# Performance work log

Hardware: AMD Instinct MI355X
Metric: run time of the kernel (lower is better)

Reference implementation:

```python
import jax, jax.numpy as jnp
import numpy as np

N = 50000
E = 800000
NUM_GRAPHS = 64
D_IN = 261
D_SAGE = 64
D_LIN = 32
N_SAGE_REST = 6
N_LIN_REST = 3
EPS = 1e-5


def _layernorm(x, g, b):
    mu = jnp.mean(x, axis=-1, keepdims=True)
    var = jnp.mean((x - mu) ** 2, axis=-1, keepdims=True)
    return (x - mu) * jax.lax.rsqrt(var + EPS) * g + b


def _sage_block(x, Wl, bl, Wr, g, b, src, dst, inv_deg, residual):
    # mean aggregation of neighbor (source) features onto targets
    msum = jax.ops.segment_sum(x[src], dst, num_segments=N)  # [N, d]
    mean = msum * inv_deg  # [N, d]
    f = mean @ Wl + bl + x @ Wr  # lin_l(aggr) + lin_r(x); lin_r has no bias
    f = jax.nn.gelu(f, approximate=False)
    f = _layernorm(f, g, b)
    if residual:
        f = f + x
    return f


def _lin_block(x, W, b, g, beta, residual):
    f = jax.nn.gelu(x @ W + b, approximate=False)
    f = _layernorm(f, g, beta)
    if residual:
        f = f + x
    return f


def setup_inputs() -> dict:
    key = jax.random.key(0)
    ks = jax.random.split(key, 24)
    x = jax.random.normal(ks[0], (N, D_IN), dtype=jnp.float32)
    edge_index = jax.random.randint(ks[1], (2, E), 0, N, dtype=jnp.int64)
    batch = jnp.sort(jax.random.randint(ks[2], (N,), 0, NUM_GRAPHS, dtype=jnp.int64))

    def glorot(k, shape):
        fan_in = shape[0]
        return jax.random.normal(k, shape, dtype=jnp.float32) / np.sqrt(fan_in)

    inp = {
        "x": x, "edge_index": edge_index, "batch": batch,
        # first SAGE block (261 -> 64, no residual)
        "Wl0": glorot(ks[3], (D_IN, D_SAGE)), "bl0": jnp.zeros((D_SAGE,), jnp.float32),
        "Wr0": glorot(ks[4], (D_IN, D_SAGE)),
        "g0": jnp.ones((D_SAGE,), jnp.float32), "beta0": jnp.zeros((D_SAGE,), jnp.float32),
        # 6 residual SAGE blocks (64 -> 64), stacked
        "Wl": glorot(ks[5], (N_SAGE_REST, D_SAGE, D_SAGE)),
        "bl": jnp.zeros((N_SAGE_REST, D_SAGE), jnp.float32),
        "Wr": glorot(ks[6], (N_SAGE_REST, D_SAGE, D_SAGE)),
        "g": jnp.ones((N_SAGE_REST, D_SAGE), jnp.float32),
        "beta": jnp.zeros((N_SAGE_REST, D_SAGE), jnp.float32),
        # MLP: first LinearBlock 64 -> 32 (no residual)
        "M0": glorot(ks[7], (D_SAGE, D_LIN)), "mb0": jnp.zeros((D_LIN,), jnp.float32),
        "mg0": jnp.ones((D_LIN,), jnp.float32), "mbeta0": jnp.zeros((D_LIN,), jnp.float32),
        # 3 residual LinearBlocks 32 -> 32, stacked
        "M": glorot(ks[8], (N_LIN_REST, D_LIN, D_LIN)),
        "mb": jnp.zeros((N_LIN_REST, D_LIN), jnp.float32),
        "mg": jnp.ones((N_LIN_REST, D_LIN), jnp.float32),
        "mbeta": jnp.zeros((N_LIN_REST, D_LIN), jnp.float32),
        # final Linear 32 -> 1
        "Wf": glorot(ks[9], (D_LIN, 1)), "bf": jnp.zeros((1,), jnp.float32),
    }
    return inp


def reference(x, edge_index, batch, Wl0, bl0, Wr0, g0, beta0, Wl, bl, Wr, g, beta,
              M0, mb0, mg0, mbeta0, M, mb, mg, mbeta, Wf, bf):
    src, dst = edge_index[0], edge_index[1]
    deg = jax.ops.segment_sum(jnp.ones((E,), x.dtype), dst, num_segments=N)
    inv_deg = (1.0 / jnp.maximum(deg, 1.0))[:, None]  # [N,1]

    h = _sage_block(x, Wl0, bl0, Wr0, g0, beta0, src, dst, inv_deg, residual=False)
    for i in range(N_SAGE_REST):
        h = _sage_block(h, Wl[i], bl[i], Wr[i], g[i], beta[i], src, dst, inv_deg, residual=True)

    pooled = jax.ops.segment_sum(h, batch, num_segments=NUM_GRAPHS)  # [G, 64]

    m = _lin_block(pooled, M0, mb0, mg0, mbeta0, residual=False)
    for i in range(N_LIN_REST):
        m = _lin_block(m, M[i], mb[i], mg[i], mbeta[i], residual=True)
    return m @ Wf + bf  # [G, 1]
```

## Files before the change

kernel.cpp:

```cpp
#include <hip/hip_runtime.h>
#include <hip/hip_bf16.h>
#include <math.h>

#define N_NODES 50000
#define N_EDGES 800000
#define NUM_GRAPHS 64
#define NPAD 50048
#define KPAD0 288
#define PSPLIT 16
#define MAXDEG 64

#define GEMM0_GRID (NPAD / 64)
#define LAYER_GRID (NPAD / 32)
#define ZERO_GRID  ((N_NODES + 255) / 256)
#define PREPW_TOT  (128 * KPAD0 + 6 * 128 * 64)
#define PREPW_GRID ((PREPW_TOT + 255) / 256)

#define SLICES 8
#define NPS 6250
#define SCHUNK 2048
#define SCHUNKS ((N_EDGES + SCHUNK - 1) / SCHUNK)
#define SCAT_GRID (SCHUNKS * SLICES)
#define CONV_GRID (NPAD * (KPAD0 / 8) / 256)

typedef __attribute__((ext_vector_type(8))) short short8;
typedef __attribute__((ext_vector_type(4))) float f32x4;

__device__ __forceinline__ float gelu_f(float v) {
    return 0.5f * v * (1.0f + erff(v * 0.70710678118654752440f));
}

__device__ __forceinline__ float half_sum32(float v) {
    v += __shfl_xor(v, 1); v += __shfl_xor(v, 2); v += __shfl_xor(v, 4);
    v += __shfl_xor(v, 8); v += __shfl_xor(v, 16);
    return v;
}

__device__ __forceinline__ float group_sum8(float v) {
    v += __shfl_xor(v, 1); v += __shfl_xor(v, 2); v += __shfl_xor(v, 4);
    return v;
}

__device__ __forceinline__ unsigned short f2bf(float f) {
    unsigned int u = __float_as_uint(f);
    unsigned int r = (u + 0x7fffu + ((u >> 16) & 1u)) >> 16;
    return (unsigned short)r;
}

__device__ __forceinline__ float bf_lo(unsigned int u) {
    return __uint_as_float(u << 16);
}
__device__ __forceinline__ float bf_hi(unsigned int u) {
    return __uint_as_float(u & 0xffff0000u);
}


__global__ void k_prep(int* __restrict__ deg,
                       const float* __restrict__ Wl0, const float* __restrict__ Wr0,
                       const float* __restrict__ Wl, const float* __restrict__ Wr,
                       unsigned short* __restrict__ Bt0, unsigned short* __restrict__ BtR) {
    const int blk = blockIdx.x, tid = threadIdx.x;
    if (blk < ZERO_GRID) {
        int i = blk * 256 + tid;
        if (i < N_NODES) deg[i] = 0;
        return;
    }
    int idx = (blk - ZERO_GRID) * 256 + tid;
    const int n0 = 128 * KPAD0;
    if (idx < n0) {
        int j = idx / KPAD0, k = idx - j * KPAD0;
        float v = 0.0f;
        if (k < 261) v = (j < 64) ? Wl0[k * 64 + j] : Wr0[k * 64 + (j - 64)];
        Bt0[idx] = f2bf(v);
    } else if (idx < PREPW_TOT) {
        int r = idx - n0;
        int l = r >> 13;
        int rr = r & 8191;
        int j = rr >> 6, k = rr & 63;
        float v = (j < 64) ? Wl[l * 4096 + k * 64 + j] : Wr[l * 4096 + k * 64 + (j - 64)];
        BtR[r] = f2bf(v);
    }
}


__global__ __launch_bounds__(256) void k_scat(
        const int* __restrict__ src, const int* __restrict__ dst,
        int* __restrict__ deg, unsigned short* __restrict__ col64,
        const float* __restrict__ X, unsigned short* __restrict__ Xbf) {
    const int blk = blockIdx.x;
    const int tid = threadIdx.x;
    if (blk < SCAT_GRID) {
        const int s = blk & (SLICES - 1);
        const int c = blk >> 3;
        const int base = c * SCHUNK;
        const int lim = min(base + SCHUNK, N_EDGES);
        for (int i = base + tid; i < lim; i += 256) {
            int d = dst[i];
            int sv = src[i];
            if (d / NPS == s) {
                int pos = atomicAdd(&deg[d], 1);
                if (pos < MAXDEG) col64[(d << 6) + pos] = (unsigned short)sv;
            }
        }
    } else {
        int t = (blk - SCAT_GRID) * 256 + tid;
        int node = t / (KPAD0 / 8);
        int k8 = (t - node * (KPAD0 / 8)) * 8;
        short8 v8;
        if (node < N_NODES) {
            #pragma unroll
            for (int j = 0; j < 8; ++j) {
                int k = k8 + j;
                float val = (k < 261) ? X[(size_t)node * 261 + k] : 0.0f;
                v8[j] = (short)f2bf(val);
            }
        } else {
            #pragma unroll
            for (int j = 0; j < 8; ++j) v8[j] = 0;
        }
        *(short8*)&Xbf[(size_t)node * KPAD0 + k8] = v8;
    }
}


__global__ __launch_bounds__(256) void k_gemm0(
        const unsigned short* __restrict__ Xbf, const unsigned short* __restrict__ Bt0,
        unsigned short* __restrict__ U, float* __restrict__ V) {
    const int tid = threadIdx.x;
    const int lane = tid & 63, wid = tid >> 6;
    const int l16 = lane & 15, quad = lane >> 4;
    const int m0 = blockIdx.x * 64;
    f32x4 acc[8];
    #pragma unroll
    for (int j = 0; j < 8; ++j) { acc[j][0] = 0.f; acc[j][1] = 0.f; acc[j][2] = 0.f; acc[j][3] = 0.f; }
    const unsigned short* xr = Xbf + (size_t)(m0 + wid * 16 + l16) * KPAD0 + quad * 8;
    const unsigned short* br = Bt0 + (size_t)l16 * KPAD0 + quad * 8;
    for (int kc = 0; kc < KPAD0; kc += 32) {
        short8 af = *(const short8*)(xr + kc);
        #pragma unroll
        for (int j = 0; j < 8; ++j) {
            short8 bfv = *(const short8*)(br + (size_t)j * 16 * KPAD0 + kc);
            acc[j] = __builtin_amdgcn_mfma_f32_16x16x32_bf16(af, bfv, acc[j], 0, 0, 0);
        }
    }
    const int rbase = m0 + wid * 16 + quad * 4;
    #pragma unroll
    for (int j = 0; j < 4; ++j)
        #pragma unroll
        for (int r = 0; r < 4; ++r)
            U[(size_t)(rbase + r) * 64 + j * 16 + l16] = f2bf(acc[j][r]);
    #pragma unroll
    for (int j = 4; j < 8; ++j)
        #pragma unroll
        for (int r = 0; r < 4; ++r)
            V[(size_t)(rbase + r) * 64 + (j - 4) * 16 + l16] = acc[j][r];
}


__global__ __launch_bounds__(256) void k_layer(
        const unsigned short* __restrict__ U_in, const float* __restrict__ V_in,
        unsigned short* __restrict__ h,
        float* __restrict__ hf_out,
        const int* __restrict__ deg, const unsigned short* __restrict__ col64,
        const float* __restrict__ bias, const float* __restrict__ gam,
        const float* __restrict__ bet,
        const unsigned short* __restrict__ Bt_next,
        unsigned short* __restrict__ U_out, float* __restrict__ V_out,
        int residual, int have_gemm) {
    __shared__ __align__(16) unsigned short sA[2 * 32 * 32];
    const int tid = threadIdx.x;
    const int lane = tid & 63, wid = tid >> 6;
    const int sub = lane >> 3, hl = lane & 7;
    const int base = lane & 56;
    const int m0 = blockIdx.x * 32;
    const uint4* __restrict__ Up = (const uint4*)U_in;

    const int nl = wid * 8 + sub;
    const int node = m0 + nl;
    const bool valid = (node < N_NODES);
    const int nd = valid ? node : 0;
    const int dg = valid ? deg[nd] : 0;
    const int cnt = min(dg, MAXDEG);
    uint4 cv = make_uint4(0u, 0u, 0u, 0u);
    if (valid) cv = *(const uint4*)&col64[((size_t)nd << 6) + hl * 8];
    float s0 = 0.f, s1 = 0.f, s2 = 0.f, s3 = 0.f, s4 = 0.f, s5 = 0.f, s6 = 0.f, s7 = 0.f;
    for (int b = 0; b * 8 < cnt; b += 2) {
        #pragma unroll
        for (int hh = 0; hh < 2; ++hh) {
            const int sl = base + b + hh;
            unsigned int p0 = (unsigned int)__shfl((int)cv.x, sl);
            unsigned int p1 = (unsigned int)__shfl((int)cv.y, sl);
            unsigned int p2 = (unsigned int)__shfl((int)cv.z, sl);
            unsigned int p3 = (unsigned int)__shfl((int)cv.w, sl);
            const int eb = (b + hh) * 8;
            int c[8];
            c[0] = (int)(p0 & 0xffffu); c[1] = (int)(p0 >> 16);
            c[2] = (int)(p1 & 0xffffu); c[3] = (int)(p1 >> 16);
            c[4] = (int)(p2 & 0xffffu); c[5] = (int)(p2 >> 16);
            c[6] = (int)(p3 & 0xffffu); c[7] = (int)(p3 >> 16);
            #pragma unroll
            for (int i = 0; i < 8; ++i) {
                uint4 u = (eb + i < cnt) ? Up[(size_t)c[i] * 8 + hl] : make_uint4(0u, 0u, 0u, 0u);
                s0 += bf_lo(u.x); s1 += bf_hi(u.x);
                s2 += bf_lo(u.y); s3 += bf_hi(u.y);
                s4 += bf_lo(u.z); s5 += bf_hi(u.z);
                s6 += bf_lo(u.w); s7 += bf_hi(u.w);
            }
        }
    }
    const float id = 1.0f / fmaxf((float)dg, 1.0f);
    const float4 b0 = *(const float4*)&bias[8 * hl];
    const float4 b1 = *(const float4*)&bias[8 * hl + 4];
    float4 v0 = make_float4(0.f, 0.f, 0.f, 0.f), v1 = v0;
    if (valid) {
        v0 = *(const float4*)&V_in[(size_t)nd * 64 + 8 * hl];
        v1 = *(const float4*)&V_in[(size_t)nd * 64 + 8 * hl + 4];
    }
    float f0 = gelu_f(s0 * id + b0.x + v0.x);
    float f1 = gelu_f(s1 * id + b0.y + v0.y);
    float f2 = gelu_f(s2 * id + b0.z + v0.z);
    float f3 = gelu_f(s3 * id + b0.w + v0.w);
    float f4 = gelu_f(s4 * id + b1.x + v1.x);
    float f5 = gelu_f(s5 * id + b1.y + v1.y);
    float f6 = gelu_f(s6 * id + b1.z + v1.z);
    float f7 = gelu_f(s7 * id + b1.w + v1.w);
    float mu = group_sum8(((f0 + f1) + (f2 + f3)) + ((f4 + f5) + (f6 + f7))) * 0.015625f;
    float d0 = f0 - mu, d1 = f1 - mu, d2 = f2 - mu, d3 = f3 - mu;
    float d4 = f4 - mu, d5 = f5 - mu, d6 = f6 - mu, d7 = f7 - mu;
    float var = group_sum8(((d0 * d0 + d1 * d1) + (d2 * d2 + d3 * d3)) +
                           ((d4 * d4 + d5 * d5) + (d6 * d6 + d7 * d7))) * 0.015625f;
    float rs = rsqrtf(var + 1e-5f);
    const float4 g0v = *(const float4*)&gam[8 * hl];
    const float4 g1v = *(const float4*)&gam[8 * hl + 4];
    const float4 e0v = *(const float4*)&bet[8 * hl];
    const float4 e1v = *(const float4*)&bet[8 * hl + 4];
    f0 = d0 * rs * g0v.x + e0v.x;
    f1 = d1 * rs * g0v.y + e0v.y;
    f2 = d2 * rs * g0v.z + e0v.z;
    f3 = d3 * rs * g0v.w + e0v.w;
    f4 = d4 * rs * g1v.x + e1v.x;
    f5 = d5 * rs * g1v.y + e1v.y;
    f6 = d6 * rs * g1v.z + e1v.z;
    f7 = d7 * rs * g1v.w + e1v.w;
    if (residual && valid) {
        uint4 hu = ((const uint4*)h)[(size_t)nd * 8 + hl];
        f0 += bf_lo(hu.x); f1 += bf_hi(hu.x);
        f2 += bf_lo(hu.y); f3 += bf_hi(hu.y);
        f4 += bf_lo(hu.z); f5 += bf_hi(hu.z);
        f6 += bf_lo(hu.w); f7 += bf_hi(hu.w);
    }
    uint4 outw;
    outw.x = (unsigned int)f2bf(f0) | ((unsigned int)f2bf(f1) << 16);
    outw.y = (unsigned int)f2bf(f2) | ((unsigned int)f2bf(f3) << 16);
    outw.z = (unsigned int)f2bf(f4) | ((unsigned int)f2bf(f5) << 16);
    outw.w = (unsigned int)f2bf(f6) | ((unsigned int)f2bf(f7) << 16);
    if (valid) {
        ((uint4*)h)[(size_t)nd * 8 + hl] = outw;
        if (hf_out) {
            *(float4*)&hf_out[(size_t)nd * 64 + 8 * hl] = make_float4(f0, f1, f2, f3);
            *(float4*)&hf_out[(size_t)nd * 64 + 8 * hl + 4] = make_float4(f4, f5, f6, f7);
        }
    }
    *(uint4*)&sA[(((hl >> 2) * 32 + nl) << 5) + (hl & 3) * 8] = outw;

    if (!have_gemm) return;
    __syncthreads();

    const int l16 = lane & 15, quad = lane >> 4;
    const int wrow = wid & 1, colh = wid >> 1;
    f32x4 acc[4];
    #pragma unroll
    for (int j = 0; j < 4; ++j) { acc[j][0] = 0.f; acc[j][1] = 0.f; acc[j][2] = 0.f; acc[j][3] = 0.f; }
    #pragma unroll
    for (int kc = 0; kc < 64; kc += 32) {
        short8 af = *(const short8*)&sA[(((kc >> 5) * 32 + wrow * 16 + l16) << 5) + quad * 8];
        #pragma unroll
        for (int j = 0; j < 4; ++j) {
            short8 bfv = *(const short8*)&Bt_next[(size_t)(colh * 64 + j * 16 + l16) * 64 + kc + quad * 8];
            acc[j] = __builtin_amdgcn_mfma_f32_16x16x32_bf16(af, bfv, acc[j], 0, 0, 0);
        }
    }
    const int rbase = m0 + wrow * 16 + quad * 4;
    if (colh == 0) {
        #pragma unroll
        for (int j = 0; j < 4; ++j)
            #pragma unroll
            for (int r = 0; r < 4; ++r)
                U_out[(size_t)(rbase + r) * 64 + j * 16 + l16] = f2bf(acc[j][r]);
    } else {
        #pragma unroll
        for (int j = 0; j < 4; ++j)
            #pragma unroll
            for (int r = 0; r < 4; ++r)
                V_out[(size_t)(rbase + r) * 64 + j * 16 + l16] = acc[j][r];
    }
}


__global__ __launch_bounds__(256) void k_pool1(const float* __restrict__ h, const int* __restrict__ batch,
                                               float* __restrict__ partial, int n) {
    __shared__ float sred[4][64];
    const int g = blockIdx.x / PSPLIT;
    const int s = blockIdx.x - g * PSPLIT;
    const int lane = threadIdx.x & 63, wid = threadIdx.x >> 6;
    int lo = 0, hi = n;
    while (lo < hi) { int mid = (lo + hi) >> 1; if (batch[mid] < g) lo = mid + 1; else hi = mid; }
    const int start = lo;
    lo = 0; hi = n;
    while (lo < hi) { int mid = (lo + hi) >> 1; if (batch[mid] < g + 1) lo = mid + 1; else hi = mid; }
    const int end = lo;
    const int len = end - start;
    const int chunk = (len + PSPLIT - 1) / PSPLIT;
    const int a = start + s * chunk;
    const int b = min(a + chunk, end);
    float sum = 0.0f;
    for (int node = a + wid; node < b; node += 4) sum += h[(size_t)node * 64 + lane];
    sred[wid][lane] = sum;
    __syncthreads();
    if (wid == 0)
        partial[(size_t)blockIdx.x * 64 + lane] = sred[0][lane] + sred[1][lane] + sred[2][lane] + sred[3][lane];
}


__global__ __launch_bounds__(1024) void k_head(const float* __restrict__ partial,
                                               const float* __restrict__ M0, const float* __restrict__ mb0,
                                               const float* __restrict__ mg0, const float* __restrict__ mbeta0,
                                               const float* __restrict__ M, const float* __restrict__ mb,
                                               const float* __restrict__ mg, const float* __restrict__ mbeta,
                                               const float* __restrict__ Wf, const float* __restrict__ bf,
                                               float* __restrict__ out) {
    __shared__ float sP[64 * 64];
    __shared__ float sA[64 * 33];
    __shared__ float sB[64 * 33];
    const int tx = threadIdx.x, ty = threadIdx.y;
    const int tid = ty * 32 + tx;
    for (int i = tid; i < 64 * 64; i += 1024) {
        int g = i >> 6, f = i & 63;
        float s = 0.0f;
        #pragma unroll
        for (int s2 = 0; s2 < PSPLIT; ++s2) s += partial[(size_t)(g * PSPLIT + s2) * 64 + f];
        sP[i] = s;
    }
    __syncthreads();
    #pragma unroll
    for (int rr = 0; rr < 2; ++rr) {
        int r = ty + rr * 32;
        float a = mb0[tx];
        for (int k = 0; k < 64; ++k) a += sP[r * 64 + k] * M0[k * 32 + tx];
        a = gelu_f(a);
        float mu = half_sum32(a) * (1.0f / 32.0f);
        float d = a - mu;
        float var = half_sum32(d * d) * (1.0f / 32.0f);
        a = d * rsqrtf(var + 1e-5f) * mg0[tx] + mbeta0[tx];
        sA[r * 33 + tx] = a;
    }
    __syncthreads();
    float* cur = sA;
    float* nxt = sB;
    for (int L = 0; L < 3; ++L) {
        const float* Mi = M + L * 32 * 32;
        const float* mbi = mb + L * 32;
        const float* mgi = mg + L * 32;
        const float* mbetai = mbeta + L * 32;
        #pragma unroll
        for (int rr = 0; rr < 2; ++rr) {
            int r = ty + rr * 32;
            float a = mbi[tx];
            for (int k = 0; k < 32; ++k) a += cur[r * 33 + k] * Mi[k * 32 + tx];
            a = gelu_f(a);
            float mu = half_sum32(a) * (1.0f / 32.0f);
            float d = a - mu;
            float var = half_sum32(d * d) * (1.0f / 32.0f);
            a = d * rsqrtf(var + 1e-5f) * mgi[tx] + mbetai[tx] + cur[r * 33 + tx];
            nxt[r * 33 + tx] = a;
        }
        __syncthreads();
        float* t = cur; cur = nxt; nxt = t;
    }
    #pragma unroll
    for (int rr = 0; rr < 2; ++rr) {
        int r = ty + rr * 32;
        float p = cur[r * 33 + tx] * Wf[tx];
        p = half_sum32(p);
        if (tx == 0) out[r] = p + bf[0];
    }
}


extern "C" void kernel_launch(void* const* d_in, const int* in_sizes, int n_in,
                              void* d_out, int out_size, void* d_ws, size_t ws_size,
                              hipStream_t stream) {
    const int N = N_NODES;
    const int E = N_EDGES;

    const float* x    = (const float*)d_in[0];
    const int* eidx   = (const int*)d_in[1];
    const int* batch  = (const int*)d_in[2];
    const float* Wl0  = (const float*)d_in[3];
    const float* bl0  = (const float*)d_in[4];
    const float* Wr0  = (const float*)d_in[5];
    const float* g0   = (const float*)d_in[6];
    const float* bet0 = (const float*)d_in[7];
    const float* Wl   = (const float*)d_in[8];
    const float* bl   = (const float*)d_in[9];
    const float* Wr   = (const float*)d_in[10];
    const float* gR   = (const float*)d_in[11];
    const float* betR = (const float*)d_in[12];
    const float* M0   = (const float*)d_in[13];
    const float* mb0  = (const float*)d_in[14];
    const float* mg0  = (const float*)d_in[15];
    const float* mbe0 = (const float*)d_in[16];
    const float* M    = (const float*)d_in[17];
    const float* mb   = (const float*)d_in[18];
    const float* mg   = (const float*)d_in[19];
    const float* mbe  = (const float*)d_in[20];
    const float* Wf   = (const float*)d_in[21];
    const float* bf   = (const float*)d_in[22];

    const int* src = eidx;
    const int* dst = eidx + E;

    char* p = (char*)d_ws;
    auto alloc = [&](size_t bytes) -> void* {
        void* q = (void*)p;
        p += (bytes + 255) & ~(size_t)255;
        return q;
    };
    int*   deg    = (int*)alloc((size_t)N * 4);
    unsigned short* col64 = (unsigned short*)alloc((size_t)N * MAXDEG * 2);
    unsigned short* Bt0 = (unsigned short*)alloc((size_t)128 * KPAD0 * 2);
    unsigned short* BtR = (unsigned short*)alloc((size_t)6 * 128 * 64 * 2);
    unsigned short* Xbf = (unsigned short*)alloc((size_t)NPAD * KPAD0 * 2);
    unsigned short* Ua  = (unsigned short*)alloc((size_t)NPAD * 64 * 2);
    unsigned short* Ub  = (unsigned short*)alloc((size_t)NPAD * 64 * 2);
    float* Va   = (float*)alloc((size_t)NPAD * 64 * 4);
    float* Vb   = (float*)alloc((size_t)NPAD * 64 * 4);
    unsigned short* hbuf = (unsigned short*)alloc((size_t)NPAD * 64 * 2);
    float* partial = (float*)alloc((size_t)NUM_GRAPHS * PSPLIT * 64 * 4);

    k_prep<<<ZERO_GRID + PREPW_GRID, 256, 0, stream>>>(deg, Wl0, Wr0, Wl, Wr, Bt0, BtR);

    k_scat<<<SCAT_GRID + CONV_GRID, 256, 0, stream>>>(src, dst, deg, col64, x, Xbf);

    k_gemm0<<<GEMM0_GRID, 256, 0, stream>>>(Xbf, Bt0, Ua, Va);

    unsigned short* Uin = Ua;  float* Vin = Va;
    unsigned short* Uout = Ub; float* Vout = Vb;
    for (int i = 0; i < 7; ++i) {
        const float* bias = (i == 0) ? bl0  : bl  + (size_t)(i - 1) * 64;
        const float* gam  = (i == 0) ? g0   : gR  + (size_t)(i - 1) * 64;
        const float* bet  = (i == 0) ? bet0 : betR + (size_t)(i - 1) * 64;
        const int have_gemm = (i < 6);
        float* hf = (i == 6) ? Vout : nullptr;
        k_layer<<<LAYER_GRID, 256, 0, stream>>>(
            Uin, Vin, hbuf, hf, deg, col64, bias, gam, bet,
            have_gemm ? (BtR + (size_t)i * 128 * 64) : BtR,
            Uout, Vout, (i > 0) ? 1 : 0, have_gemm);
        unsigned short* tu = Uin; Uin = Uout; Uout = tu;
        float* tv = Vin; Vin = Vout; Vout = tv;
    }
    float* hf_final = Vin;

    k_pool1<<<NUM_GRAPHS * PSPLIT, 256, 0, stream>>>(hf_final, batch, partial, N);
    k_head<<<1, dim3(32, 32), 0, stream>>>(partial, M0, mb0, mg0, mbe0, M, mb, mg, mbe, Wf, bf, (float*)d_out);
}
```

Before: 402.2 us.

## Stage GEMM weights in LDS, split gemm0 by output half, move X conversion

The first GEMM kernel now splits each 64-row tile across two blocks, one computing the U half and one the V half. Each block stages its 64x288 bf16 weight slice in padded shared memory instead of reading B fragments from global memory. The per-layer kernel likewise stages the 128x64 next-layer weights into padded LDS before the aggregation. The X-to-bf16 conversion moves from the scatter kernel into the prep kernel, and the scatter loop now loads src only for edges in its slice. The cost is extra LDS use (about 37KB in gemm0), which may lower occupancy, and X rows are re-read by both gemm0 halves.

```diff
diff --git a/kernel.cpp b/kernel.cpp
--- a/kernel.cpp
+++ b/kernel.cpp
@@ -10,18 +10,18 @@
 #define PSPLIT 16
 #define MAXDEG 64
 
-#define GEMM0_GRID (NPAD / 64)
+#define G0_GRID    (NPAD / 32)
 #define LAYER_GRID (NPAD / 32)
 #define ZERO_GRID  ((N_NODES + 255) / 256)
 #define PREPW_TOT  (128 * KPAD0 + 6 * 128 * 64)
 #define PREPW_GRID ((PREPW_TOT + 255) / 256)
+#define CONV_GRID  (NPAD * (KPAD0 / 8) / 256)
 
 #define SLICES 8
 #define NPS 6250
 #define SCHUNK 2048
 #define SCHUNKS ((N_EDGES + SCHUNK - 1) / SCHUNK)
 #define SCAT_GRID (SCHUNKS * SLICES)
-#define CONV_GRID (NPAD * (KPAD0 / 8) / 256)
 
 typedef __attribute__((ext_vector_type(8))) short short8;
 typedef __attribute__((ext_vector_type(4))) float f32x4;
@@ -58,67 +58,65 @@
 __global__ void k_prep(int* __restrict__ deg,
                        const float* __restrict__ Wl0, const float* __restrict__ Wr0,
                        const float* __restrict__ Wl, const float* __restrict__ Wr,
-                       unsigned short* __restrict__ Bt0, unsigned short* __restrict__ BtR) {
+                       unsigned short* __restrict__ Bt0, unsigned short* __restrict__ BtR,
+                       const float* __restrict__ X, unsigned short* __restrict__ Xbf) {
     const int blk = blockIdx.x, tid = threadIdx.x;
     if (blk < ZERO_GRID) {
         int i = blk * 256 + tid;
         if (i < N_NODES) deg[i] = 0;
         return;
     }
-    int idx = (blk - ZERO_GRID) * 256 + tid;
-    const int n0 = 128 * KPAD0;
-    if (idx < n0) {
-        int j = idx / KPAD0, k = idx - j * KPAD0;
-        float v = 0.0f;
-        if (k < 261) v = (j < 64) ? Wl0[k * 64 + j] : Wr0[k * 64 + (j - 64)];
-        Bt0[idx] = f2bf(v);
-    } else if (idx < PREPW_TOT) {
-        int r = idx - n0;
-        int l = r >> 13;
-        int rr = r & 8191;
-        int j = rr >> 6, k = rr & 63;
-        float v = (j < 64) ? Wl[l * 4096 + k * 64 + j] : Wr[l * 4096 + k * 64 + (j - 64)];
-        BtR[r] = f2bf(v);
-    }
+    if (blk < ZERO_GRID + PREPW_GRID) {
+        int idx = (blk - ZERO_GRID) * 256 + tid;
+        const int n0 = 128 * KPAD0;
+        if (idx < n0) {
+            int j = idx / KPAD0, k = idx - j * KPAD0;
+            float v = 0.0f;
+            if (k < 261) v = (j < 64) ? Wl0[k * 64 + j] : Wr0[k * 64 + (j - 64)];
+            Bt0[idx] = f2bf(v);
+        } else if (idx < PREPW_TOT) {
+            int r = idx - n0;
+            int l = r >> 13;
+            int rr = r & 8191;
+            int j = rr >> 6, k = rr & 63;
+            float v = (j < 64) ? Wl[l * 4096 + k * 64 + j] : Wr[l * 4096 + k * 64 + (j - 64)];
+            BtR[r] = f2bf(v);
+        }
+        return;
+    }
+    int t = (blk - ZERO_GRID - PREPW_GRID) * 256 + tid;
+    int node = t / (KPAD0 / 8);
+    int k8 = (t - node * (KPAD0 / 8)) * 8;
+    short8 v8;
+    if (node < N_NODES) {
+        #pragma unroll
+        for (int j = 0; j < 8; ++j) {
+            int k = k8 + j;
+            float val = (k < 261) ? X[(size_t)node * 261 + k] : 0.0f;
+            v8[j] = (short)f2bf(val);
+        }
+    } else {
+        #pragma unroll
+        for (int j = 0; j < 8; ++j) v8[j] = 0;
+    }
+    *(short8*)&Xbf[(size_t)node * KPAD0 + k8] = v8;
 }
 
 
 __global__ __launch_bounds__(256) void k_scat(
         const int* __restrict__ src, const int* __restrict__ dst,
-        int* __restrict__ deg, unsigned short* __restrict__ col64,
-        const float* __restrict__ X, unsigned short* __restrict__ Xbf) {
-    const int blk = blockIdx.x;
-    const int tid = threadIdx.x;
-    if (blk < SCAT_GRID) {
-        const int s = blk & (SLICES - 1);
-        const int c = blk >> 3;
-        const int base = c * SCHUNK;
-        const int lim = min(base + SCHUNK, N_EDGES);
-        for (int i = base + tid; i < lim; i += 256) {
-            int d = dst[i];
+        int* __restrict__ deg, unsigned short* __restrict__ col64) {
+    const int s = blockIdx.x & (SLICES - 1);
+    const int c = blockIdx.x >> 3;
+    const int base = c * SCHUNK;
+    const int lim = min(base + SCHUNK, N_EDGES);
+    for (int i = base + (int)threadIdx.x; i < lim; i += 256) {
+        int d = dst[i];
+        if (d / NPS == s) {
             int sv = src[i];
-            if (d / NPS == s) {
-                int pos = atomicAdd(&deg[d], 1);
-                if (pos < MAXDEG) col64[(d << 6) + pos] = (unsigned short)sv;
-            }
-        }
-    } else {
-        int t = (blk - SCAT_GRID) * 256 + tid;
-        int node = t / (KPAD0 / 8);
-        int k8 = (t - node * (KPAD0 / 8)) * 8;
-        short8 v8;
-        if (node < N_NODES) {
-            #pragma unroll
-            for (int j = 0; j < 8; ++j) {
-                int k = k8 + j;
-                float val = (k < 261) ? X[(size_t)node * 261 + k] : 0.0f;
-                v8[j] = (short)f2bf(val);
-            }
-        } else {
-            #pragma unroll
-            for (int j = 0; j < 8; ++j) v8[j] = 0;
-        }
-        *(short8*)&Xbf[(size_t)node * KPAD0 + k8] = v8;
+            int pos = atomicAdd(&deg[d], 1);
+            if (pos < MAXDEG) col64[(d << 6) + pos] = (unsigned short)sv;
+        }
     }
 }
 
@@ -126,34 +124,47 @@
 __global__ __launch_bounds__(256) void k_gemm0(
         const unsigned short* __restrict__ Xbf, const unsigned short* __restrict__ Bt0,
         unsigned short* __restrict__ U, float* __restrict__ V) {
+    __shared__ __align__(16) unsigned short sB[64 * 296];
     const int tid = threadIdx.x;
     const int lane = tid & 63, wid = tid >> 6;
     const int l16 = lane & 15, quad = lane >> 4;
-    const int m0 = blockIdx.x * 64;
-    f32x4 acc[8];
-    #pragma unroll
-    for (int j = 0; j < 8; ++j) { acc[j][0] = 0.f; acc[j][1] = 0.f; acc[j][2] = 0.f; acc[j][3] = 0.f; }
+    const int ch = blockIdx.x & 1;
+    const int m0 = (blockIdx.x >> 1) * 64;
+    #pragma unroll
+    for (int k = 0; k < 9; ++k) {
+        int g = k * 256 + tid;
+        int row = g / 36;
+        int part = (g - row * 36) * 8;
+        *(short8*)&sB[row * 296 + part] =
+            *(const short8*)&Bt0[(size_t)(ch * 64 + row) * KPAD0 + part];
+    }
+    f32x4 acc[4];
+    #pragma unroll
+    for (int j = 0; j < 4; ++j) { acc[j][0] = 0.f; acc[j][1] = 0.f; acc[j][2] = 0.f; acc[j][3] = 0.f; }
     const unsigned short* xr = Xbf + (size_t)(m0 + wid * 16 + l16) * KPAD0 + quad * 8;
-    const unsigned short* br = Bt0 + (size_t)l16 * KPAD0 + quad * 8;
+    __syncthreads();
     for (int kc = 0; kc < KPAD0; kc += 32) {
         short8 af = *(const short8*)(xr + kc);
         #pragma unroll
-        for (int j = 0; j < 8; ++j) {
-            short8 bfv = *(const short8*)(br + (size_t)j * 16 * KPAD0 + kc);
+        for (int j = 0; j < 4; ++j) {
+            short8 bfv = *(const short8*)&sB[(j * 16 + l16) * 296 + kc + quad * 8];
             acc[j] = __builtin_amdgcn_mfma_f32_16x16x32_bf16(af, bfv, acc[j], 0, 0, 0);
         }
     }
     const int rbase = m0 + wid * 16 + quad * 4;
-    #pragma unroll
-    for (int j = 0; j < 4; ++j)
-        #pragma unroll
-        for (int r = 0; r < 4; ++r)
-            U[(size_t)(rbase + r) * 64 + j * 16 + l16] = f2bf(acc[j][r]);
-    #pragma unroll
-    for (int j = 4; j < 8; ++j)
-        #pragma unroll
-        for (int r = 0; r < 4; ++r)
-            V[(size_t)(rbase + r) * 64 + (j - 4) * 16 + l16] = acc[j][r];
+    if (ch == 0) {
+        #pragma unroll
+        for (int j = 0; j < 4; ++j)
+            #pragma unroll
+            for (int r = 0; r < 4; ++r)
+                U[(size_t)(rbase + r) * 64 + j * 16 + l16] = f2bf(acc[j][r]);
+    } else {
+        #pragma unroll
+        for (int j = 0; j < 4; ++j)
+            #pragma unroll
+            for (int r = 0; r < 4; ++r)
+                V[(size_t)(rbase + r) * 64 + j * 16 + l16] = acc[j][r];
+    }
 }
 
 
@@ -168,12 +179,22 @@
         unsigned short* __restrict__ U_out, float* __restrict__ V_out,
         int residual, int have_gemm) {
     __shared__ __align__(16) unsigned short sA[2 * 32 * 32];
+    __shared__ __align__(16) unsigned short sB[128 * 72];
     const int tid = threadIdx.x;
     const int lane = tid & 63, wid = tid >> 6;
     const int sub = lane >> 3, hl = lane & 7;
     const int base = lane & 56;
     const int m0 = blockIdx.x * 32;
     const uint4* __restrict__ Up = (const uint4*)U_in;
+
+    if (have_gemm) {
+        #pragma unroll
+        for (int k = 0; k < 4; ++k) {
+            int g = k * 256 + tid;
+            int row = g >> 3, part = (g & 7) * 8;
+            *(short8*)&sB[row * 72 + part] = *(const short8*)&Bt_next[(size_t)row * 64 + part];
+        }
+    }
 
     const int nl = wid * 8 + sub;
     const int node = m0 + nl;
@@ -276,7 +297,7 @@
         short8 af = *(const short8*)&sA[(((kc >> 5) * 32 + wrow * 16 + l16) << 5) + quad * 8];
         #pragma unroll
         for (int j = 0; j < 4; ++j) {
-            short8 bfv = *(const short8*)&Bt_next[(size_t)(colh * 64 + j * 16 + l16) * 64 + kc + quad * 8];
+            short8 bfv = *(const short8*)&sB[(colh * 64 + j * 16 + l16) * 72 + kc + quad * 8];
             acc[j] = __builtin_amdgcn_mfma_f32_16x16x32_bf16(af, bfv, acc[j], 0, 0, 0);
         }
     }
@@ -438,11 +459,12 @@
     unsigned short* hbuf = (unsigned short*)alloc((size_t)NPAD * 64 * 2);
     float* partial = (float*)alloc((size_t)NUM_GRAPHS * PSPLIT * 64 * 4);
 
-    k_prep<<<ZERO_GRID + PREPW_GRID, 256, 0, stream>>>(deg, Wl0, Wr0, Wl, Wr, Bt0, BtR);
-
-    k_scat<<<SCAT_GRID + CONV_GRID, 256, 0, stream>>>(src, dst, deg, col64, x, Xbf);
-
-    k_gemm0<<<GEMM0_GRID, 256, 0, stream>>>(Xbf, Bt0, Ua, Va);
+    k_prep<<<ZERO_GRID + PREPW_GRID + CONV_GRID, 256, 0, stream>>>(
+        deg, Wl0, Wr0, Wl, Wr, Bt0, BtR, x, Xbf);
+
+    k_scat<<<SCAT_GRID, 256, 0, stream>>>(src, dst, deg, col64);
+
+    k_gemm0<<<G0_GRID, 256, 0, stream>>>(Xbf, Bt0, Ua, Va);
 
     unsigned short* Uin = Ua;  float* Vin = Va;
     unsigned short* Uout = Ub; float* Vout = Vb;
```

New measurement: 394.7 us. No clear change (-1.9%).
